# Performance work log

Hardware: AMD Instinct MI355X
Metric: run time of the kernel (lower is better)

The kernel has to match this reference:

```python
import jax, jax.numpy as jnp
import numpy as np

B, T, C, H = 2, 2048, 1024, 16
D = C // H


def setup_inputs() -> dict:
    key = jax.random.key(0)
    k1, k2, k3 = jax.random.split(key, 3)
    x = jax.random.normal(k1, (B, T, C), dtype=jnp.float32)
    w_attn = jax.random.normal(k2, (3 * C, C), dtype=jnp.float32) * (1.0 / np.sqrt(C))
    w_proj = jax.random.normal(k3, (C, C), dtype=jnp.float32) * (1.0 / np.sqrt(C))
    # causal mask, 1 = keep, 0 = masked (matches att.masked_fill(mask == 0, -inf))
    mask = jnp.tril(jnp.ones((T, T), dtype=jnp.int32))[None, None, :, :]
    return {"x": x, "w_attn": w_attn, "w_proj": w_proj, "mask": mask}


def reference(x, w_attn, w_proj, mask):
    Bq, Tq, Cq = x.shape
    qkv = x @ w_attn.T                      # [B,T,3C] (torch Linear: x @ W^T)
    q, k, v = jnp.split(qkv, 3, axis=2)
    # [B,T,C] -> [B,H,T,D]
    q = q.reshape(Bq, Tq, H, D).transpose(0, 2, 1, 3)
    k = k.reshape(Bq, Tq, H, D).transpose(0, 2, 1, 3)
    v = v.reshape(Bq, Tq, H, D).transpose(0, 2, 1, 3)
    att = jnp.einsum("bhqd,bhkd->bhqk", q, k) * (1.0 / np.sqrt(D))
    att = jnp.where(mask == 0, -jnp.inf, att)
    att = jax.nn.softmax(att, axis=-1)      # dropout p=0.0 -> identity
    y = jnp.einsum("bhqk,bhkd->bhqd", att, v)
    y = y.transpose(0, 2, 1, 3).reshape(Bq, Tq, Cq)
    return y @ w_proj.T
```

## Files before the change

kernel.cpp:

```cpp
#include <hip/hip_runtime.h>
#include <hip/hip_bf16.h>
#include <math.h>


typedef __attribute__((ext_vector_type(4))) float floatx4;
typedef __attribute__((ext_vector_type(8))) __bf16 bf16x8;

#define MFMA_BF16(a, b, c) __builtin_amdgcn_mfma_f32_16x16x32_bf16((a), (b), (c), 0, 0, 0)

typedef __attribute__((address_space(1))) const uint32_t* gas_t;
typedef __attribute__((address_space(3))) uint32_t* las_t;
__device__ inline void gl2lds16(const void* g, void* l) {
    __builtin_amdgcn_global_load_lds((gas_t)g, (las_t)l, 16, 0, 0);
}

__device__ inline uint4 cvt8_f32_bf16(const float4 a, const float4 b) {
    union { __hip_bfloat16 h[8]; uint4 u; } c;
    c.h[0] = __float2bfloat16(a.x); c.h[1] = __float2bfloat16(a.y);
    c.h[2] = __float2bfloat16(a.z); c.h[3] = __float2bfloat16(a.w);
    c.h[4] = __float2bfloat16(b.x); c.h[5] = __float2bfloat16(b.y);
    c.h[6] = __float2bfloat16(b.z); c.h[7] = __float2bfloat16(b.w);
    return c.u;
}

__global__ __launch_bounds__(256) void cvt_f32_bf16_k(
    const float* __restrict__ in, __hip_bfloat16* __restrict__ out, int n)
{
    const int i = (blockIdx.x * 256 + threadIdx.x) * 8;
    if (i < n) {
        const float4 a = *(const float4*)&in[i];
        const float4 b = *(const float4*)&in[i + 4];
        *(uint4*)&out[i] = cvt8_f32_bf16(a, b);
    }
}

template<bool C_F32, bool QSCALE>
__global__ __launch_bounds__(256) void gemm_bt_mfma(
    const __hip_bfloat16* __restrict__ A,
    const __hip_bfloat16* __restrict__ Bt,
    void* __restrict__ Cv, int M, int N, int K)
{
    __shared__ __hip_bfloat16 As0[128][32];
    __shared__ __hip_bfloat16 As1[128][32];
    __shared__ __hip_bfloat16 Bs0[128][32];
    __shared__ __hip_bfloat16 Bs1[128][32];

    const int tid  = threadIdx.x;
    const int wave = tid >> 6;
    const int lane = tid & 63;
    const int quad = lane >> 4;
    const int l15  = lane & 15;
    const int wrow = wave >> 1;
    const int wcol = wave & 1;
    const int bm = blockIdx.y * 128;
    const int bn = blockIdx.x * 128;

    floatx4 acc[4][4];
#pragma unroll
    for (int i = 0; i < 4; ++i)
#pragma unroll
        for (int j = 0; j < 4; ++j)
            acc[i][j] = (floatx4){0.f, 0.f, 0.f, 0.f};

    const int srow = lane >> 2;
    const int scol = (lane & 3) * 8;

    const __hip_bfloat16* Abase = A  + (size_t)bm * K;
    const __hip_bfloat16* Bbase = Bt + (size_t)bn * K;

    for (int k0 = 0; k0 < K; k0 += 64) {
#pragma unroll
        for (int c = 0; c < 2; ++c) {
            const int rbase = wave * 32 + c * 16;
            const size_t ga = (size_t)(rbase + srow) * K + k0 + scol;
            gl2lds16(&Abase[ga],      &As0[rbase][0]);
            gl2lds16(&Abase[ga + 32], &As1[rbase][0]);
            gl2lds16(&Bbase[ga],      &Bs0[rbase][0]);
            gl2lds16(&Bbase[ga + 32], &Bs1[rbase][0]);
        }
        __syncthreads();

#pragma unroll
        for (int kd = 0; kd < 2; ++kd) {
            const __hip_bfloat16 (*Ap)[32] = kd ? As1 : As0;
            const __hip_bfloat16 (*Bp)[32] = kd ? Bs1 : Bs0;
            bf16x8 af[4], bfv[4];
#pragma unroll
            for (int i = 0; i < 4; ++i)
                af[i] = *(const bf16x8*)&Ap[wrow * 64 + i * 16 + l15][quad * 8];
#pragma unroll
            for (int j = 0; j < 4; ++j)
                bfv[j] = *(const bf16x8*)&Bp[wcol * 64 + j * 16 + l15][quad * 8];
#pragma unroll
            for (int i = 0; i < 4; ++i)
#pragma unroll
                for (int j = 0; j < 4; ++j)
                    acc[i][j] = MFMA_BF16(af[i], bfv[j], acc[i][j]);
        }
        __syncthreads();
    }

    const float sc = (QSCALE && bn < 1024) ? 0.18033688f : 1.0f;

#pragma unroll
    for (int i = 0; i < 4; ++i)
#pragma unroll
        for (int j = 0; j < 4; ++j)
#pragma unroll
            for (int r = 0; r < 4; ++r) {
                const int row = bm + wrow * 64 + i * 16 + quad * 4 + r;
                const int col = bn + wcol * 64 + j * 16 + l15;
                if (C_F32)
                    ((float*)Cv)[(size_t)row * N + col] = acc[i][j][r];
                else
                    ((__hip_bfloat16*)Cv)[(size_t)row * N + col] =
                        __float2bfloat16(acc[i][j][r] * sc);
            }
}

__global__ __launch_bounds__(256) void gemm_bt_mfma_n64(
    const __hip_bfloat16* __restrict__ A,
    const __hip_bfloat16* __restrict__ Bt,
    float* __restrict__ C, int M, int N, int K)
{
    __shared__ __hip_bfloat16 As[128][32];
    __shared__ __hip_bfloat16 Bs[64][32];

    const int tid  = threadIdx.x;
    const int wave = tid >> 6;
    const int lane = tid & 63;
    const int quad = lane >> 4;
    const int l15  = lane & 15;
    const int wrow = wave >> 1;
    const int wcol = wave & 1;
    const int bm = blockIdx.y * 128;
    const int bn = blockIdx.x * 64;

    floatx4 acc[4][2];
#pragma unroll
    for (int i = 0; i < 4; ++i)
#pragma unroll
        for (int j = 0; j < 2; ++j)
            acc[i][j] = (floatx4){0.f, 0.f, 0.f, 0.f};

    const int srow = lane >> 2;
    const int scol = (lane & 3) * 8;

    const __hip_bfloat16* Abase = A  + (size_t)bm * K;
    const __hip_bfloat16* Bbase = Bt + (size_t)bn * K;

    for (int k0 = 0; k0 < K; k0 += 32) {
        {
            const int ra0 = wave * 32;
            gl2lds16(&Abase[(size_t)(ra0 + srow) * K + k0 + scol], &As[ra0][0]);
            gl2lds16(&Abase[(size_t)(ra0 + 16 + srow) * K + k0 + scol], &As[ra0 + 16][0]);
            const int rb0 = wave * 16;
            gl2lds16(&Bbase[(size_t)(rb0 + srow) * K + k0 + scol], &Bs[rb0][0]);
        }
        __syncthreads();

        bf16x8 af[4], bfv[2];
#pragma unroll
        for (int i = 0; i < 4; ++i)
            af[i] = *(const bf16x8*)&As[wrow * 64 + i * 16 + l15][quad * 8];
#pragma unroll
        for (int j = 0; j < 2; ++j)
            bfv[j] = *(const bf16x8*)&Bs[wcol * 32 + j * 16 + l15][quad * 8];

#pragma unroll
        for (int i = 0; i < 4; ++i)
#pragma unroll
            for (int j = 0; j < 2; ++j)
                acc[i][j] = MFMA_BF16(af[i], bfv[j], acc[i][j]);
        __syncthreads();
    }

#pragma unroll
    for (int i = 0; i < 4; ++i)
#pragma unroll
        for (int j = 0; j < 2; ++j)
#pragma unroll
            for (int r = 0; r < 4; ++r) {
                const int row = bm + wrow * 64 + i * 16 + quad * 4 + r;
                const int col = bn + wcol * 32 + j * 16 + l15;
                C[(size_t)row * N + col] = acc[i][j][r];
            }
}

__global__ __launch_bounds__(256) void transpose_v(
    const __hip_bfloat16* __restrict__ qkv, __hip_bfloat16* __restrict__ VtT)
{
    __shared__ __hip_bfloat16 Ls[64][72];
    const int b = blockIdx.z, h = blockIdx.y, t0 = blockIdx.x * 64;
    const int tid = threadIdx.x;
    {
        const int r = tid >> 2, c = (tid & 3) * 16;
        const size_t g = ((size_t)(b * 2048 + t0 + r)) * 3072 + 2048 + h * 64 + c;
        *(uint4*)&Ls[r][c]     = *(const uint4*)&qkv[g];
        *(uint4*)&Ls[r][c + 8] = *(const uint4*)&qkv[g + 8];
    }
    __syncthreads();
    {
        const int d = tid >> 2, k0 = (tid & 3) * 16;
        __hip_bfloat16 tmp[16];
#pragma unroll
        for (int j = 0; j < 16; ++j) tmp[j] = Ls[k0 + j][d];
        const size_t g = ((size_t)((b * 16 + h) * 64 + d)) * 2048 + t0 + k0;
        *(uint4*)&VtT[g]     = *(uint4*)&tmp[0];
        *(uint4*)&VtT[g + 8] = *(uint4*)&tmp[8];
    }
}

__global__ __launch_bounds__(256) void attn_kernel(
    const __hip_bfloat16* __restrict__ qkv,
    const __hip_bfloat16* __restrict__ VtT,
    __hip_bfloat16* __restrict__ y)
{
    constexpr int T = 2048;
    __shared__ __hip_bfloat16 Ks[64][72];
    __shared__ __hip_bfloat16 Vt[64][72];
    __shared__ __hip_bfloat16 PsA[64][72];
    __shared__ __hip_bfloat16 PsB[64][72];

    const int bh = blockIdx.x;
    const int b = bh >> 4, h = bh & 15;
    const int p = blockIdx.y;
    const int q0A = p * 64;
    const int q0B = (31 - p) * 64;

    const int tid  = threadIdx.x;
    const int wave = tid >> 6;
    const int lane = tid & 63;
    const int quad = lane >> 4;
    const int l15  = lane & 15;

    const __hip_bfloat16* base  = qkv + (size_t)b * T * 3072;
    const __hip_bfloat16* vbase = VtT + (size_t)((b * 16 + h) * 64) * 2048;

    bf16x8 aqA[2], aqB[2];
#pragma unroll
    for (int kd = 0; kd < 2; ++kd) {
        aqA[kd] = *(const bf16x8*)&base[(size_t)(q0A + wave * 16 + l15) * 3072 + h * 64 + kd * 32 + quad * 8];
        aqB[kd] = *(const bf16x8*)&base[(size_t)(q0B + wave * 16 + l15) * 3072 + h * 64 + kd * 32 + quad * 8];
    }

    bf16x8 ones;
#pragma unroll
    for (int i = 0; i < 8; ++i) ones[i] = (__bf16)1.0f;

    floatx4 accA[4], accB[4], lA, lB;
#pragma unroll
    for (int r = 0; r < 4; ++r) {
        accA[r] = (floatx4){0.f, 0.f, 0.f, 0.f};
        accB[r] = (floatx4){0.f, 0.f, 0.f, 0.f};
    }
    lA = (floatx4){0.f, 0.f, 0.f, 0.f};
    lB = (floatx4){0.f, 0.f, 0.f, 0.f};

    const int sr = tid >> 2;
    const int sc = (tid & 3) * 16;

    for (int j0 = 0; j0 <= q0B; j0 += 64) {
        const bool actA = (j0 <= q0A);
        const bool dgA  = (j0 == q0A);
        const bool dgB  = (j0 == q0B);

        {
            const size_t kg = (size_t)(j0 + sr) * 3072 + 1024 + h * 64 + sc;
            *(uint4*)&Ks[sr][sc]     = *(const uint4*)&base[kg];
            *(uint4*)&Ks[sr][sc + 8] = *(const uint4*)&base[kg + 8];
            const size_t vg = (size_t)sr * 2048 + j0 + sc;
            *(uint4*)&Vt[sr][sc]     = *(const uint4*)&vbase[vg];
            *(uint4*)&Vt[sr][sc + 8] = *(const uint4*)&vbase[vg + 8];
        }
        __syncthreads();

        floatx4 sA[4], sB[4];
#pragma unroll
        for (int jt = 0; jt < 4; ++jt) {
            sA[jt] = (floatx4){0.f, 0.f, 0.f, 0.f};
            sB[jt] = (floatx4){0.f, 0.f, 0.f, 0.f};
        }
#pragma unroll
        for (int jt = 0; jt < 4; ++jt)
#pragma unroll
            for (int kd = 0; kd < 2; ++kd) {
                bf16x8 bk = *(const bf16x8*)&Ks[jt * 16 + l15][kd * 32 + quad * 8];
                sB[jt] = MFMA_BF16(aqB[kd], bk, sB[jt]);
                if (actA) sA[jt] = MFMA_BF16(aqA[kd], bk, sA[jt]);
            }

        const int myrow = wave * 16 + quad * 4;
#pragma unroll
        for (int jt = 0; jt < 4; ++jt) {
            const int col = jt * 16 + l15;
#pragma unroll
            for (int r = 0; r < 4; ++r) {
                float pv = __builtin_amdgcn_exp2f(sB[jt][r]);
                if (dgB && col > (myrow + r)) pv = 0.f;
                PsB[myrow + r][col] = __float2bfloat16(pv);
            }
            if (actA) {
#pragma unroll
                for (int r = 0; r < 4; ++r) {
                    float pv = __builtin_amdgcn_exp2f(sA[jt][r]);
                    if (dgA && col > (myrow + r)) pv = 0.f;
                    PsA[myrow + r][col] = __float2bfloat16(pv);
                }
            }
        }
        __syncthreads();

#pragma unroll
        for (int kk = 0; kk < 2; ++kk) {
            bf16x8 apB = *(const bf16x8*)&PsB[wave * 16 + l15][kk * 32 + quad * 8];
            bf16x8 apA;
            if (actA) apA = *(const bf16x8*)&PsA[wave * 16 + l15][kk * 32 + quad * 8];
            lB = MFMA_BF16(apB, ones, lB);
            if (actA) lA = MFMA_BF16(apA, ones, lA);
#pragma unroll
            for (int jd = 0; jd < 4; ++jd) {
                bf16x8 bv = *(const bf16x8*)&Vt[jd * 16 + l15][kk * 32 + quad * 8];
                accB[jd] = MFMA_BF16(apB, bv, accB[jd]);
                if (actA) accA[jd] = MFMA_BF16(apA, bv, accA[jd]);
            }
        }
        __syncthreads();
    }

    float invA[4], invB[4];
#pragma unroll
    for (int r = 0; r < 4; ++r) { invA[r] = 1.f / lA[r]; invB[r] = 1.f / lB[r]; }
#pragma unroll
    for (int jd = 0; jd < 4; ++jd)
#pragma unroll
        for (int r = 0; r < 4; ++r) {
            const int col = h * 64 + jd * 16 + l15;
            const int rowA = q0A + wave * 16 + quad * 4 + r;
            y[((size_t)b * T + rowA) * 1024 + col] = __float2bfloat16(accA[jd][r] * invA[r]);
            const int rowB = q0B + wave * 16 + quad * 4 + r;
            y[((size_t)b * T + rowB) * 1024 + col] = __float2bfloat16(accB[jd][r] * invB[r]);
        }
}

extern "C" void kernel_launch(void* const* d_in, const int* in_sizes, int n_in,
                              void* d_out, int out_size, void* d_ws, size_t ws_size,
                              hipStream_t stream)
{
    const float* x      = (const float*)d_in[0];
    const float* w_attn = (const float*)d_in[1];
    const float* w_proj = (const float*)d_in[2];

    float* out = (float*)d_out;
    __hip_bfloat16* xb  = (__hip_bfloat16*)d_ws;
    __hip_bfloat16* wab = xb  + (size_t)4096 * 1024;
    __hip_bfloat16* wpb = wab + (size_t)3072 * 1024;
    __hip_bfloat16* qkv = wpb + (size_t)1024 * 1024;
    __hip_bfloat16* y   = qkv + (size_t)4096 * 3072;
    __hip_bfloat16* vt  = y   + (size_t)4096 * 1024;

    cvt_f32_bf16_k<<<2048, 256, 0, stream>>>(x,      xb,  4096 * 1024);
    cvt_f32_bf16_k<<<1536, 256, 0, stream>>>(w_attn, wab, 3072 * 1024);
    cvt_f32_bf16_k<<<512,  256, 0, stream>>>(w_proj, wpb, 1024 * 1024);

    gemm_bt_mfma<false, true><<<dim3(24, 32), 256, 0, stream>>>(xb, wab, qkv, 4096, 3072, 1024);

    transpose_v<<<dim3(32, 16, 2), 256, 0, stream>>>(qkv, vt);
    attn_kernel<<<dim3(32, 16), 256, 0, stream>>>(qkv, vt, y);

    gemm_bt_mfma_n64<<<dim3(16, 32), 256, 0, stream>>>(y, wpb, out, 4096, 1024, 1024);
}
```

Measured before the change: 223.0 us.

## Split attention KV range across two blocks, fuse V transpose into QKV GEMM

Attention now uses a third grid dimension: each block handles every other 64-key tile, so there are twice as many blocks. Each block writes unnormalized fp32 partial outputs and row sums, and a new combine kernel adds the two halves and normalizes. The QKV GEMM epilogue writes V directly in transposed layout, which removes the separate transpose kernel. The three conversion launches are merged into one. These changes are meant to improve GPU occupancy and cut launch count, at the cost of extra fp32 partial-buffer traffic and one more kernel.

```diff
diff --git a/kernel.cpp b/kernel.cpp
--- a/kernel.cpp
+++ b/kernel.cpp
@@ -23,22 +23,25 @@
     return c.u;
 }
 
-__global__ __launch_bounds__(256) void cvt_f32_bf16_k(
-    const float* __restrict__ in, __hip_bfloat16* __restrict__ out, int n)
-{
-    const int i = (blockIdx.x * 256 + threadIdx.x) * 8;
-    if (i < n) {
-        const float4 a = *(const float4*)&in[i];
-        const float4 b = *(const float4*)&in[i + 4];
-        *(uint4*)&out[i] = cvt8_f32_bf16(a, b);
-    }
-}
-
-template<bool C_F32, bool QSCALE>
-__global__ __launch_bounds__(256) void gemm_bt_mfma(
+__global__ __launch_bounds__(256) void cvt_all(
+    const float* __restrict__ x, const float* __restrict__ wa,
+    const float* __restrict__ wp, __hip_bfloat16* __restrict__ out)
+{
+    const size_t e = ((size_t)blockIdx.x * 256 + threadIdx.x) * 8;
+    const float* src; size_t off;
+    if (e < 4194304)      { src = x;  off = e; }
+    else if (e < 7340032) { src = wa; off = e - 4194304; }
+    else                  { src = wp; off = e - 7340032; }
+    const float4 a = *(const float4*)&src[off];
+    const float4 b = *(const float4*)&src[off + 4];
+    *(uint4*)&out[e] = cvt8_f32_bf16(a, b);
+}
+
+__global__ __launch_bounds__(256) void gemm_qkv(
     const __hip_bfloat16* __restrict__ A,
     const __hip_bfloat16* __restrict__ Bt,
-    void* __restrict__ Cv, int M, int N, int K)
+    __hip_bfloat16* __restrict__ qk,
+    __hip_bfloat16* __restrict__ vt, int K)
 {
     __shared__ __hip_bfloat16 As0[128][32];
     __shared__ __hip_bfloat16 As1[128][32];
@@ -100,22 +103,32 @@
         __syncthreads();
     }
 
-    const float sc = (QSCALE && bn < 1024) ? 0.18033688f : 1.0f;
-
-#pragma unroll
-    for (int i = 0; i < 4; ++i)
-#pragma unroll
-        for (int j = 0; j < 4; ++j)
-#pragma unroll
-            for (int r = 0; r < 4; ++r) {
-                const int row = bm + wrow * 64 + i * 16 + quad * 4 + r;
-                const int col = bn + wcol * 64 + j * 16 + l15;
-                if (C_F32)
-                    ((float*)Cv)[(size_t)row * N + col] = acc[i][j][r];
-                else
-                    ((__hip_bfloat16*)Cv)[(size_t)row * N + col] =
-                        __float2bfloat16(acc[i][j][r] * sc);
-            }
+    if (bn < 2048) {
+        const float sc = (bn < 1024) ? 0.18033688f : 1.0f;
+#pragma unroll
+        for (int i = 0; i < 4; ++i)
+#pragma unroll
+            for (int j = 0; j < 4; ++j)
+#pragma unroll
+                for (int r = 0; r < 4; ++r) {
+                    const int row = bm + wrow * 64 + i * 16 + quad * 4 + r;
+                    const int col = bn + wcol * 64 + j * 16 + l15;
+                    qk[(size_t)row * 2048 + col] = __float2bfloat16(acc[i][j][r] * sc);
+                }
+    } else {
+#pragma unroll
+        for (int i = 0; i < 4; ++i)
+#pragma unroll
+            for (int j = 0; j < 4; ++j) {
+                const int trow0 = bm + wrow * 64 + i * 16 + quad * 4;
+                const int d = bn - 2048 + wcol * 64 + j * 16 + l15;
+                const int b = trow0 >> 11, t0 = trow0 & 2047;
+                union { __hip_bfloat16 h[4]; uint2 u; } pk;
+#pragma unroll
+                for (int r = 0; r < 4; ++r) pk.h[r] = __float2bfloat16(acc[i][j][r]);
+                *(uint2*)&vt[((size_t)(b * 16 + (d >> 6)) * 64 + (d & 63)) * 2048 + t0] = pk.u;
+            }
+    }
 }
 
 __global__ __launch_bounds__(256) void gemm_bt_mfma_n64(
@@ -187,34 +200,10 @@
             }
 }
 
-__global__ __launch_bounds__(256) void transpose_v(
-    const __hip_bfloat16* __restrict__ qkv, __hip_bfloat16* __restrict__ VtT)
-{
-    __shared__ __hip_bfloat16 Ls[64][72];
-    const int b = blockIdx.z, h = blockIdx.y, t0 = blockIdx.x * 64;
-    const int tid = threadIdx.x;
-    {
-        const int r = tid >> 2, c = (tid & 3) * 16;
-        const size_t g = ((size_t)(b * 2048 + t0 + r)) * 3072 + 2048 + h * 64 + c;
-        *(uint4*)&Ls[r][c]     = *(const uint4*)&qkv[g];
-        *(uint4*)&Ls[r][c + 8] = *(const uint4*)&qkv[g + 8];
-    }
-    __syncthreads();
-    {
-        const int d = tid >> 2, k0 = (tid & 3) * 16;
-        __hip_bfloat16 tmp[16];
-#pragma unroll
-        for (int j = 0; j < 16; ++j) tmp[j] = Ls[k0 + j][d];
-        const size_t g = ((size_t)((b * 16 + h) * 64 + d)) * 2048 + t0 + k0;
-        *(uint4*)&VtT[g]     = *(uint4*)&tmp[0];
-        *(uint4*)&VtT[g + 8] = *(uint4*)&tmp[8];
-    }
-}
-
 __global__ __launch_bounds__(256) void attn_kernel(
-    const __hip_bfloat16* __restrict__ qkv,
-    const __hip_bfloat16* __restrict__ VtT,
-    __hip_bfloat16* __restrict__ y)
+    const __hip_bfloat16* __restrict__ qk,
+    const __hip_bfloat16* __restrict__ vt,
+    float* __restrict__ part)
 {
     constexpr int T = 2048;
     __shared__ __hip_bfloat16 Ks[64][72];
@@ -225,6 +214,7 @@
     const int bh = blockIdx.x;
     const int b = bh >> 4, h = bh & 15;
     const int p = blockIdx.y;
+    const int s = blockIdx.z;
     const int q0A = p * 64;
     const int q0B = (31 - p) * 64;
 
@@ -234,14 +224,14 @@
     const int quad = lane >> 4;
     const int l15  = lane & 15;
 
-    const __hip_bfloat16* base  = qkv + (size_t)b * T * 3072;
-    const __hip_bfloat16* vbase = VtT + (size_t)((b * 16 + h) * 64) * 2048;
+    const __hip_bfloat16* base  = qk + (size_t)b * T * 2048;
+    const __hip_bfloat16* vbase = vt + (size_t)((b * 16 + h) * 64) * 2048;
 
     bf16x8 aqA[2], aqB[2];
 #pragma unroll
     for (int kd = 0; kd < 2; ++kd) {
-        aqA[kd] = *(const bf16x8*)&base[(size_t)(q0A + wave * 16 + l15) * 3072 + h * 64 + kd * 32 + quad * 8];
-        aqB[kd] = *(const bf16x8*)&base[(size_t)(q0B + wave * 16 + l15) * 3072 + h * 64 + kd * 32 + quad * 8];
+        aqA[kd] = *(const bf16x8*)&base[(size_t)(q0A + wave * 16 + l15) * 2048 + h * 64 + kd * 32 + quad * 8];
+        aqB[kd] = *(const bf16x8*)&base[(size_t)(q0B + wave * 16 + l15) * 2048 + h * 64 + kd * 32 + quad * 8];
     }
 
     bf16x8 ones;
@@ -260,13 +250,13 @@
     const int sr = tid >> 2;
     const int sc = (tid & 3) * 16;
 
-    for (int j0 = 0; j0 <= q0B; j0 += 64) {
+    for (int j0 = s * 64; j0 <= q0B; j0 += 128) {
         const bool actA = (j0 <= q0A);
         const bool dgA  = (j0 == q0A);
         const bool dgB  = (j0 == q0B);
 
         {
-            const size_t kg = (size_t)(j0 + sr) * 3072 + 1024 + h * 64 + sc;
+            const size_t kg = (size_t)(j0 + sr) * 2048 + 1024 + h * 64 + sc;
             *(uint4*)&Ks[sr][sc]     = *(const uint4*)&base[kg];
             *(uint4*)&Ks[sr][sc + 8] = *(const uint4*)&base[kg + 8];
             const size_t vg = (size_t)sr * 2048 + j0 + sc;
@@ -328,19 +318,57 @@
         __syncthreads();
     }
 
-    float invA[4], invB[4];
-#pragma unroll
-    for (int r = 0; r < 4; ++r) { invA[r] = 1.f / lA[r]; invB[r] = 1.f / lB[r]; }
+    float* pA = part + (size_t)((s * 32 + bh) * 32 + p) * 4160;
+    float* pB = part + (size_t)((s * 32 + bh) * 32 + (31 - p)) * 4160;
 #pragma unroll
     for (int jd = 0; jd < 4; ++jd)
 #pragma unroll
         for (int r = 0; r < 4; ++r) {
-            const int col = h * 64 + jd * 16 + l15;
-            const int rowA = q0A + wave * 16 + quad * 4 + r;
-            y[((size_t)b * T + rowA) * 1024 + col] = __float2bfloat16(accA[jd][r] * invA[r]);
-            const int rowB = q0B + wave * 16 + quad * 4 + r;
-            y[((size_t)b * T + rowB) * 1024 + col] = __float2bfloat16(accB[jd][r] * invB[r]);
-        }
+            const int row = wave * 16 + quad * 4 + r;
+            const int col = jd * 16 + l15;
+            pA[row * 64 + col] = accA[jd][r];
+            pB[row * 64 + col] = accB[jd][r];
+        }
+    if (l15 == 0) {
+#pragma unroll
+        for (int r = 0; r < 4; ++r) {
+            const int row = wave * 16 + quad * 4 + r;
+            pA[4096 + row] = lA[r];
+            pB[4096 + row] = lB[r];
+        }
+    }
+}
+
+__global__ __launch_bounds__(256) void combine_kernel(
+    const float* __restrict__ part, __hip_bfloat16* __restrict__ y)
+{
+    const int bh = blockIdx.x, t = blockIdx.y;
+    const int b = bh >> 4, h = bh & 15;
+    const float* p0 = part + (size_t)((0 * 32 + bh) * 32 + t) * 4160;
+    const float* p1 = part + (size_t)((1 * 32 + bh) * 32 + t) * 4160;
+
+    __shared__ float linv[64];
+    const int tid = threadIdx.x;
+    if (tid < 64) linv[tid] = 1.f / (p0[4096 + tid] + p1[4096 + tid]);
+    __syncthreads();
+
+    const int row = tid >> 2;
+    const int c0  = (tid & 3) * 16;
+    const float inv = linv[row];
+
+    union { __hip_bfloat16 h[16]; uint4 u[2]; } ob;
+#pragma unroll
+    for (int c = 0; c < 4; ++c) {
+        const float4 a = *(const float4*)&p0[row * 64 + c0 + c * 4];
+        const float4 d = *(const float4*)&p1[row * 64 + c0 + c * 4];
+        ob.h[c * 4 + 0] = __float2bfloat16((a.x + d.x) * inv);
+        ob.h[c * 4 + 1] = __float2bfloat16((a.y + d.y) * inv);
+        ob.h[c * 4 + 2] = __float2bfloat16((a.z + d.z) * inv);
+        ob.h[c * 4 + 3] = __float2bfloat16((a.w + d.w) * inv);
+    }
+    __hip_bfloat16* yp = &y[((size_t)(b * 2048 + t * 64 + row)) * 1024 + h * 64 + c0];
+    *(uint4*)(yp)     = ob.u[0];
+    *(uint4*)(yp + 8) = ob.u[1];
 }
 
 extern "C" void kernel_launch(void* const* d_in, const int* in_sizes, int n_in,
@@ -355,18 +383,17 @@
     __hip_bfloat16* xb  = (__hip_bfloat16*)d_ws;
     __hip_bfloat16* wab = xb  + (size_t)4096 * 1024;
     __hip_bfloat16* wpb = wab + (size_t)3072 * 1024;
-    __hip_bfloat16* qkv = wpb + (size_t)1024 * 1024;
-    __hip_bfloat16* y   = qkv + (size_t)4096 * 3072;
+    __hip_bfloat16* qkb = wpb + (size_t)1024 * 1024;
+    __hip_bfloat16* y   = qkb + (size_t)4096 * 2048;
     __hip_bfloat16* vt  = y   + (size_t)4096 * 1024;
-
-    cvt_f32_bf16_k<<<2048, 256, 0, stream>>>(x,      xb,  4096 * 1024);
-    cvt_f32_bf16_k<<<1536, 256, 0, stream>>>(w_attn, wab, 3072 * 1024);
-    cvt_f32_bf16_k<<<512,  256, 0, stream>>>(w_proj, wpb, 1024 * 1024);
-
-    gemm_bt_mfma<false, true><<<dim3(24, 32), 256, 0, stream>>>(xb, wab, qkv, 4096, 3072, 1024);
-
-    transpose_v<<<dim3(32, 16, 2), 256, 0, stream>>>(qkv, vt);
-    attn_kernel<<<dim3(32, 16), 256, 0, stream>>>(qkv, vt, y);
+    float*          prt = (float*)(vt + (size_t)2048 * 2048);
+
+    cvt_all<<<4096, 256, 0, stream>>>(x, w_attn, w_proj, xb);
+
+    gemm_qkv<<<dim3(24, 32), 256, 0, stream>>>(xb, wab, qkb, vt, 1024);
+
+    attn_kernel<<<dim3(32, 16, 2), 256, 0, stream>>>(qkb, vt, prt);
+    combine_kernel<<<dim3(32, 32), 256, 0, stream>>>(prt, y);
 
     gemm_bt_mfma_n64<<<dim3(16, 32), 256, 0, stream>>>(y, wpb, out, 4096, 1024, 1024);
 }
```

Result: faster. 209.7 us (-6.0%).
